# Optimization experiments

Hardware: AMD Instinct MI355X
Metric: run time of the kernel (lower is better)

The kernel has to match this reference:

```python
import jax, jax.numpy as jnp
import numpy as np

NEG_INF = -1e30


def setup_inputs() -> dict:
    key = jax.random.key(0)
    k1, k2, k3 = jax.random.split(key, 3)
    B, H, HKV, S, D = 2, 16, 4, 2048, 128
    q = jax.random.normal(k1, (B, H, S, D), dtype=jnp.float32)
    k = jax.random.normal(k2, (B, HKV, S, D), dtype=jnp.float32)
    v = jax.random.normal(k3, (B, HKV, S, D), dtype=jnp.float32)
    return {"q": q, "k": k, "v": v}


def reference(q, k, v):
    # Flash attention math (exact, non-tiled reference): causal + sliding-window
    # masked softmax(QK^T * scale) V with GQA head grouping.
    B, H, M, D = q.shape
    _, HKV, N, _ = k.shape
    G = H // HKV  # num_kv_groups
    W = 512       # sliding window size
    scale = 1.0 / jnp.sqrt(jnp.float32(D))

    qg = q.reshape(B, HKV, G, M, D)
    # scores: [B, HKV, G, M, N]
    scores = jnp.einsum("bkgmd,bknd->bkgmn", qg, k) * scale

    i = jnp.arange(M)[:, None]
    j = jnp.arange(N)[None, :]
    # causal: j <= i ; sliding window: only last W keys visible (i - j < W)
    keep = (j <= i) & ((i - j) < W)
    scores = jnp.where(keep[None, None, None], scores, NEG_INF)

    p = jax.nn.softmax(scores.astype(jnp.float32), axis=-1).astype(q.dtype)
    out = jnp.einsum("bkgmn,bknd->bkgmd", p, v)
    return out.reshape(B, H, M, D)
```

## Files before the change

kernel.cpp:

```cpp
#include <hip/hip_runtime.h>
#include <hip/hip_bf16.h>
#include <stdint.h>

#define SEQ 2048
#define HD  128
#define WIN 512
#define NH  16
#define NKV 4
#define BATCH 2

typedef __attribute__((ext_vector_type(8))) short bf16x8;
typedef __attribute__((ext_vector_type(4))) float f32x4;

#define EXP2(x) __builtin_amdgcn_exp2f(x)

#define KSTR 136
#define VSTR 72
#define PSTR 72

__device__ __forceinline__ uint32_t pk2(float a, float b) {
    __hip_bfloat162 h = __float22bfloat162_rn(make_float2(a, b));
    return *reinterpret_cast<uint32_t*>(&h);
}
__device__ __forceinline__ uint16_t pk1(float a) {
    __hip_bfloat16 h = __float2bfloat16(a);
    return *reinterpret_cast<uint16_t*>(&h);
}

__global__ __launch_bounds__(256, 2) void fa_mfma(
    const float* __restrict__ q,
    const float* __restrict__ k,
    const float* __restrict__ v,
    float* __restrict__ out)
{
    const int tid  = threadIdx.x;
    const int wave = tid >> 6;
    const int lane = tid & 63;
    const int l4   = lane >> 4;
    const int l15  = lane & 15;

    const int bh   = blockIdx.x >> 4;
    const int qblk = blockIdx.x & 15;
    const int q0   = qblk << 7;
    const int hkv  = (bh & (NH - 1)) >> 2;
    const int b    = bh >> 4;

    const int i0   = q0 + wave * 32;

    __shared__ __align__(16) uint16_t lds_k[64 * KSTR];
    __shared__ __align__(16) uint16_t lds_vt[HD * VSTR];
    __shared__ __align__(16) uint16_t lds_p[4 * 32 * PSTR];
    uint16_t* pw = &lds_p[wave * 32 * PSTR];

    const float scale2 = 0.08838834764831845f * 1.4426950408889634f;

    const size_t qbase  = (size_t)bh * SEQ * HD;
    const size_t kvbase = (size_t)(b * NKV + hkv) * SEQ * HD;

    union { bf16x8 f; uint32_t u[4]; } qf[2][4];
    #pragma unroll
    for (int nt = 0; nt < 2; ++nt) {
        const float* qr = q + qbase + (size_t)(i0 + nt * 16 + l15) * HD;
        #pragma unroll
        for (int ks = 0; ks < 4; ++ks) {
            const float4* g = reinterpret_cast<const float4*>(qr + ks * 32 + l4 * 8);
            float4 a = g[0], bq = g[1];
            qf[nt][ks].u[0] = pk2(a.x * scale2, a.y * scale2);
            qf[nt][ks].u[1] = pk2(a.z * scale2, a.w * scale2);
            qf[nt][ks].u[2] = pk2(bq.x * scale2, bq.y * scale2);
            qf[nt][ks].u[3] = pk2(bq.z * scale2, bq.w * scale2);
        }
    }

    f32x4 O[2][8];
    #pragma unroll
    for (int a1 = 0; a1 < 2; ++a1)
        #pragma unroll
        for (int a2 = 0; a2 < 8; ++a2) O[a1][a2] = (f32x4){0.f, 0.f, 0.f, 0.f};
    float mrow[2] = {-1e30f, -1e30f};
    float lrow[2] = {0.f, 0.f};

    const int kt_lo_blk = (q0 >= 512) ? ((q0 - 511) >> 6) : 0;
    const int kt_hi_blk = (q0 + 127) >> 6;
    const int lo_w = (i0 >= 512) ? ((i0 - 511) >> 6) : 0;
    const int hi_w = (i0 + 31) >> 6;

    const int vdg = tid & 31;
    const int vkg = tid >> 5;
    float4 rKa[4], rKb[4], rV[8];

    auto prefetch = [&](int kt) {
        const float* kp = k + kvbase + (size_t)kt * 64 * HD;
        const float* vp = v + kvbase + (size_t)kt * 64 * HD;
        #pragma unroll
        for (int it = 0; it < 4; ++it) {
            int flat8 = tid + it * 256, key = flat8 >> 4, ch = flat8 & 15;
            const float4* g = reinterpret_cast<const float4*>(kp + key * HD + ch * 8);
            rKa[it] = g[0]; rKb[it] = g[1];
        }
        #pragma unroll
        for (int r = 0; r < 8; ++r)
            rV[r] = *reinterpret_cast<const float4*>(vp + (vkg * 8 + r) * HD + vdg * 4);
    };

    prefetch(kt_lo_blk);

    for (int kt = kt_lo_blk; kt <= kt_hi_blk; ++kt) {
        #pragma unroll
        for (int it = 0; it < 4; ++it) {
            int flat8 = tid + it * 256, key = flat8 >> 4, ch = flat8 & 15;
            uint4 wv;
            wv.x = pk2(rKa[it].x, rKa[it].y);  wv.y = pk2(rKa[it].z, rKa[it].w);
            wv.z = pk2(rKb[it].x, rKb[it].y);  wv.w = pk2(rKb[it].z, rKb[it].w);
            *reinterpret_cast<uint4*>(&lds_k[key * KSTR + ch * 8]) = wv;
        }
        {
            const float* rvf = reinterpret_cast<const float*>(rV);
            #pragma unroll
            for (int i = 0; i < 4; ++i) {
                uint4 wv;
                wv.x = pk2(rvf[0 * 4 + i], rvf[1 * 4 + i]);
                wv.y = pk2(rvf[2 * 4 + i], rvf[3 * 4 + i]);
                wv.z = pk2(rvf[4 * 4 + i], rvf[5 * 4 + i]);
                wv.w = pk2(rvf[6 * 4 + i], rvf[7 * 4 + i]);
                *reinterpret_cast<uint4*>(&lds_vt[(vdg * 4 + i) * VSTR + vkg * 8]) = wv;
            }
        }
        __syncthreads();

        if (kt < kt_hi_blk) prefetch(kt + 1);

        if (kt >= lo_w && kt <= hi_w) {
            f32x4 sf[4][2];
            #pragma unroll
            for (int mt = 0; mt < 4; ++mt) {
                #pragma unroll
                for (int nt = 0; nt < 2; ++nt) sf[mt][nt] = (f32x4){0.f, 0.f, 0.f, 0.f};
                #pragma unroll
                for (int ks = 0; ks < 4; ++ks) {
                    bf16x8 af = *reinterpret_cast<const bf16x8*>(
                        &lds_k[(mt * 16 + l15) * KSTR + ks * 32 + l4 * 8]);
                    #pragma unroll
                    for (int nt = 0; nt < 2; ++nt)
                        sf[mt][nt] = __builtin_amdgcn_mfma_f32_16x16x32_bf16(
                            af, qf[nt][ks].f, sf[mt][nt], 0, 0, 0);
                }
            }
            const bool needmask = (kt == hi_w) || (kt == lo_w && i0 > 511);
            if (needmask) {
                #pragma unroll
                for (int mt = 0; mt < 4; ++mt) {
                    int jb = kt * 64 + mt * 16 + l4 * 4;
                    #pragma unroll
                    for (int nt = 0; nt < 2; ++nt) {
                        int iq = i0 + nt * 16 + l15;
                        #pragma unroll
                        for (int r = 0; r < 4; ++r) {
                            int j = jb + r;
                            if (!((j <= iq) && (iq - j < WIN))) sf[mt][nt][r] = -1e30f;
                        }
                    }
                }
            }
            float alpha[2];
            #pragma unroll
            for (int nt = 0; nt < 2; ++nt) {
                float tm = -1e30f;
                #pragma unroll
                for (int mt = 0; mt < 4; ++mt)
                    #pragma unroll
                    for (int r = 0; r < 4; ++r) tm = fmaxf(tm, sf[mt][nt][r]);
                tm = fmaxf(tm, __shfl_xor(tm, 16, 64));
                tm = fmaxf(tm, __shfl_xor(tm, 32, 64));
                float mn = fmaxf(mrow[nt], tm);
                alpha[nt] = EXP2(mrow[nt] - mn);
                mrow[nt] = mn;
                float me = fmaxf(mn, -1e20f);
                float ts = 0.f;
                #pragma unroll
                for (int mt = 0; mt < 4; ++mt) {
                    #pragma unroll
                    for (int r = 0; r < 4; ++r) {
                        float pv = EXP2(sf[mt][nt][r] - me);
                        ts += pv;
                        pw[(nt * 16 + l15) * PSTR + mt * 16 + l4 * 4 + r] = pk1(pv);
                    }
                }
                ts += __shfl_xor(ts, 16, 64);
                ts += __shfl_xor(ts, 32, 64);
                lrow[nt] = lrow[nt] * alpha[nt] + ts;
            }
            #pragma unroll
            for (int mt = 0; mt < 2; ++mt) {
                #pragma unroll
                for (int r = 0; r < 4; ++r) {
                    float ar = __shfl(alpha[mt], l4 * 4 + r, 64);
                    #pragma unroll
                    for (int nt = 0; nt < 8; ++nt) O[mt][nt][r] *= ar;
                }
            }
            #pragma unroll
            for (int ks = 0; ks < 2; ++ks) {
                bf16x8 pa[2];
                #pragma unroll
                for (int mt = 0; mt < 2; ++mt)
                    pa[mt] = *reinterpret_cast<const bf16x8*>(
                        &pw[(mt * 16 + l15) * PSTR + ks * 32 + l4 * 8]);
                #pragma unroll
                for (int nt = 0; nt < 8; ++nt) {
                    bf16x8 vf = *reinterpret_cast<const bf16x8*>(
                        &lds_vt[(nt * 16 + l15) * VSTR + ks * 32 + l4 * 8]);
                    #pragma unroll
                    for (int mt = 0; mt < 2; ++mt)
                        O[mt][nt] = __builtin_amdgcn_mfma_f32_16x16x32_bf16(
                            pa[mt], vf, O[mt][nt], 0, 0, 0);
                }
            }
        }
        __syncthreads();
    }

    #pragma unroll
    for (int mt = 0; mt < 2; ++mt) {
        float inv = 1.0f / lrow[mt];
        #pragma unroll
        for (int r = 0; r < 4; ++r) {
            float li = __shfl(inv, l4 * 4 + r, 64);
            int row = i0 + mt * 16 + l4 * 4 + r;
            float* orow = out + qbase + (size_t)row * HD;
            #pragma unroll
            for (int nt = 0; nt < 8; ++nt)
                orow[nt * 16 + l15] = O[mt][nt][r] * li;
        }
    }
}

extern "C" void kernel_launch(void* const* d_in, const int* in_sizes, int n_in,
                              void* d_out, int out_size, void* d_ws, size_t ws_size,
                              hipStream_t stream) {
    const float* q = (const float*)d_in[0];
    const float* k = (const float*)d_in[1];
    const float* v = (const float*)d_in[2];
    float* out     = (float*)d_out;

    hipLaunchKernelGGL(fa_mfma, dim3(BATCH * NH * (SEQ / 128)), dim3(256), 0, stream,
                       q, k, v, out);
}
```

Baseline: 126.9 us.

## Double-buffer K/V in LDS, keep P in registers, defer softmax rescaling

Adds two LDS buffers for K and V^T so the next tile is packed while the current one is computed, which removes one barrier per iteration. The probability tile now stays in registers as bf16x4 fragments and feeds 16x16x16 MFMAs directly, replacing the LDS round-trip through lds_p. The O and l rescale is skipped when the new row max exceeds the running max by at most 8 in log2 units, so exponentials may reach up to 256 before normalization. The cost is double the LDS for K/V, more MFMA instructions of the smaller shape, and a small numerical-range risk from the deferred max.

After: 192.4 us. 51.5% more time.

```diff
diff --git a/kernel.cpp b/kernel.cpp
--- a/kernel.cpp
+++ b/kernel.cpp
@@ -10,21 +10,27 @@
 #define BATCH 2
 
 typedef __attribute__((ext_vector_type(8))) short bf16x8;
+typedef __attribute__((ext_vector_type(4))) short bf16x4;
 typedef __attribute__((ext_vector_type(4))) float f32x4;
 
 #define EXP2(x) __builtin_amdgcn_exp2f(x)
 
 #define KSTR 136
 #define VSTR 72
-#define PSTR 72
 
 __device__ __forceinline__ uint32_t pk2(float a, float b) {
     __hip_bfloat162 h = __float22bfloat162_rn(make_float2(a, b));
     return *reinterpret_cast<uint32_t*>(&h);
 }
-__device__ __forceinline__ uint16_t pk1(float a) {
-    __hip_bfloat16 h = __float2bfloat16(a);
-    return *reinterpret_cast<uint16_t*>(&h);
+
+__device__ __forceinline__ f32x4 mfma16(bf16x4 a, bf16x4 b, f32x4 c) {
+#if __has_builtin(__builtin_amdgcn_mfma_f32_16x16x16bf16_1k)
+    return __builtin_amdgcn_mfma_f32_16x16x16bf16_1k(a, b, c, 0, 0, 0);
+#else
+    asm volatile("v_mfma_f32_16x16x16_bf16 %0, %1, %2, %0\n\ts_nop 7\n\ts_nop 7"
+                 : "+v"(c) : "v"(a), "v"(b));
+    return c;
+#endif
 }
 
 __global__ __launch_bounds__(256, 2) void fa_mfma(
@@ -47,10 +53,8 @@
 
     const int i0   = q0 + wave * 32;
 
-    __shared__ __align__(16) uint16_t lds_k[64 * KSTR];
-    __shared__ __align__(16) uint16_t lds_vt[HD * VSTR];
-    __shared__ __align__(16) uint16_t lds_p[4 * 32 * PSTR];
-    uint16_t* pw = &lds_p[wave * 32 * PSTR];
+    __shared__ __align__(16) uint16_t lds_k[2][64 * KSTR];
+    __shared__ __align__(16) uint16_t lds_vt[2][HD * VSTR];
 
     const float scale2 = 0.08838834764831845f * 1.4426950408889634f;
 
@@ -103,32 +107,35 @@
             rV[r] = *reinterpret_cast<const float4*>(vp + (vkg * 8 + r) * HD + vdg * 4);
     };
 
-    prefetch(kt_lo_blk);
-
-    for (int kt = kt_lo_blk; kt <= kt_hi_blk; ++kt) {
+    auto pack = [&](int pb) {
         #pragma unroll
         for (int it = 0; it < 4; ++it) {
             int flat8 = tid + it * 256, key = flat8 >> 4, ch = flat8 & 15;
             uint4 wv;
             wv.x = pk2(rKa[it].x, rKa[it].y);  wv.y = pk2(rKa[it].z, rKa[it].w);
             wv.z = pk2(rKb[it].x, rKb[it].y);  wv.w = pk2(rKb[it].z, rKb[it].w);
-            *reinterpret_cast<uint4*>(&lds_k[key * KSTR + ch * 8]) = wv;
-        }
-        {
-            const float* rvf = reinterpret_cast<const float*>(rV);
-            #pragma unroll
-            for (int i = 0; i < 4; ++i) {
-                uint4 wv;
-                wv.x = pk2(rvf[0 * 4 + i], rvf[1 * 4 + i]);
-                wv.y = pk2(rvf[2 * 4 + i], rvf[3 * 4 + i]);
-                wv.z = pk2(rvf[4 * 4 + i], rvf[5 * 4 + i]);
-                wv.w = pk2(rvf[6 * 4 + i], rvf[7 * 4 + i]);
-                *reinterpret_cast<uint4*>(&lds_vt[(vdg * 4 + i) * VSTR + vkg * 8]) = wv;
-            }
-        }
-        __syncthreads();
-
-        if (kt < kt_hi_blk) prefetch(kt + 1);
+            *reinterpret_cast<uint4*>(&lds_k[pb][key * KSTR + ch * 8]) = wv;
+        }
+        const float* rvf = reinterpret_cast<const float*>(rV);
+        #pragma unroll
+        for (int i = 0; i < 4; ++i) {
+            uint4 wv;
+            wv.x = pk2(rvf[0 * 4 + i], rvf[1 * 4 + i]);
+            wv.y = pk2(rvf[2 * 4 + i], rvf[3 * 4 + i]);
+            wv.z = pk2(rvf[4 * 4 + i], rvf[5 * 4 + i]);
+            wv.w = pk2(rvf[6 * 4 + i], rvf[7 * 4 + i]);
+            *reinterpret_cast<uint4*>(&lds_vt[pb][(vdg * 4 + i) * VSTR + vkg * 8]) = wv;
+        }
+    };
+
+    prefetch(kt_lo_blk);
+    pack(0);
+    __syncthreads();
+
+    int par = 0;
+    for (int kt = kt_lo_blk; kt <= kt_hi_blk; ++kt) {
+        const bool more = (kt < kt_hi_blk);
+        if (more) prefetch(kt + 1);
 
         if (kt >= lo_w && kt <= hi_w) {
             f32x4 sf[4][2];
@@ -139,7 +146,7 @@
                 #pragma unroll
                 for (int ks = 0; ks < 4; ++ks) {
                     bf16x8 af = *reinterpret_cast<const bf16x8*>(
-                        &lds_k[(mt * 16 + l15) * KSTR + ks * 32 + l4 * 8]);
+                        &lds_k[par][(mt * 16 + l15) * KSTR + ks * 32 + l4 * 8]);
                     #pragma unroll
                     for (int nt = 0; nt < 2; ++nt)
                         sf[mt][nt] = __builtin_amdgcn_mfma_f32_16x16x32_bf16(
@@ -162,62 +169,80 @@
                     }
                 }
             }
-            float alpha[2];
+            float tm[2];
             #pragma unroll
             for (int nt = 0; nt < 2; ++nt) {
-                float tm = -1e30f;
-                #pragma unroll
-                for (int mt = 0; mt < 4; ++mt)
-                    #pragma unroll
-                    for (int r = 0; r < 4; ++r) tm = fmaxf(tm, sf[mt][nt][r]);
-                tm = fmaxf(tm, __shfl_xor(tm, 16, 64));
-                tm = fmaxf(tm, __shfl_xor(tm, 32, 64));
-                float mn = fmaxf(mrow[nt], tm);
-                alpha[nt] = EXP2(mrow[nt] - mn);
-                mrow[nt] = mn;
-                float me = fmaxf(mn, -1e20f);
-                float ts = 0.f;
-                #pragma unroll
-                for (int mt = 0; mt < 4; ++mt) {
+                float a0 = fmaxf(fmaxf(sf[0][nt][0], sf[0][nt][1]),
+                                 fmaxf(sf[0][nt][2], sf[0][nt][3]));
+                float a1 = fmaxf(fmaxf(sf[1][nt][0], sf[1][nt][1]),
+                                 fmaxf(sf[1][nt][2], sf[1][nt][3]));
+                float a2 = fmaxf(fmaxf(sf[2][nt][0], sf[2][nt][1]),
+                                 fmaxf(sf[2][nt][2], sf[2][nt][3]));
+                float a3 = fmaxf(fmaxf(sf[3][nt][0], sf[3][nt][1]),
+                                 fmaxf(sf[3][nt][2], sf[3][nt][3]));
+                float t = fmaxf(fmaxf(a0, a1), fmaxf(a2, a3));
+                t = fmaxf(t, __shfl_xor(t, 16, 64));
+                t = fmaxf(t, __shfl_xor(t, 32, 64));
+                tm[nt] = t;
+            }
+            const bool defer = __all(tm[0] <= mrow[0] + 8.0f) &&
+                               __all(tm[1] <= mrow[1] + 8.0f);
+            if (!defer) {
+                float alpha[2];
+                #pragma unroll
+                for (int nt = 0; nt < 2; ++nt) {
+                    float mn = fmaxf(mrow[nt], tm[nt]);
+                    alpha[nt] = EXP2(mrow[nt] - mn);
+                    mrow[nt] = mn;
+                    lrow[nt] *= alpha[nt];
+                }
+                #pragma unroll
+                for (int mt = 0; mt < 2; ++mt) {
                     #pragma unroll
                     for (int r = 0; r < 4; ++r) {
-                        float pv = EXP2(sf[mt][nt][r] - me);
-                        ts += pv;
-                        pw[(nt * 16 + l15) * PSTR + mt * 16 + l4 * 4 + r] = pk1(pv);
+                        float ar = __shfl(alpha[mt], l4 * 4 + r, 64);
+                        #pragma unroll
+                        for (int nt = 0; nt < 8; ++nt) O[mt][nt][r] *= ar;
                     }
                 }
+            }
+            union PF { bf16x4 v; uint32_t u[2]; };
+            PF pfrag[4][2];
+            #pragma unroll
+            for (int nt = 0; nt < 2; ++nt) {
+                float me = fmaxf(mrow[nt], -1e20f);
+                float s[4];
+                #pragma unroll
+                for (int mt = 0; mt < 4; ++mt) {
+                    float p0 = EXP2(sf[mt][nt][0] - me);
+                    float p1 = EXP2(sf[mt][nt][1] - me);
+                    float p2 = EXP2(sf[mt][nt][2] - me);
+                    float p3 = EXP2(sf[mt][nt][3] - me);
+                    pfrag[mt][nt].u[0] = pk2(p0, p1);
+                    pfrag[mt][nt].u[1] = pk2(p2, p3);
+                    s[mt] = (p0 + p1) + (p2 + p3);
+                }
+                float ts = (s[0] + s[1]) + (s[2] + s[3]);
                 ts += __shfl_xor(ts, 16, 64);
                 ts += __shfl_xor(ts, 32, 64);
-                lrow[nt] = lrow[nt] * alpha[nt] + ts;
-            }
-            #pragma unroll
-            for (int mt = 0; mt < 2; ++mt) {
-                #pragma unroll
-                for (int r = 0; r < 4; ++r) {
-                    float ar = __shfl(alpha[mt], l4 * 4 + r, 64);
-                    #pragma unroll
-                    for (int nt = 0; nt < 8; ++nt) O[mt][nt][r] *= ar;
-                }
-            }
-            #pragma unroll
-            for (int ks = 0; ks < 2; ++ks) {
-                bf16x8 pa[2];
-                #pragma unroll
-                for (int mt = 0; mt < 2; ++mt)
-                    pa[mt] = *reinterpret_cast<const bf16x8*>(
-                        &pw[(mt * 16 + l15) * PSTR + ks * 32 + l4 * 8]);
+                lrow[nt] += ts;
+            }
+            if (more) pack(par ^ 1);
+            #pragma unroll
+            for (int mt = 0; mt < 4; ++mt) {
                 #pragma unroll
                 for (int nt = 0; nt < 8; ++nt) {
-                    bf16x8 vf = *reinterpret_cast<const bf16x8*>(
-                        &lds_vt[(nt * 16 + l15) * VSTR + ks * 32 + l4 * 8]);
-                    #pragma unroll
-                    for (int mt = 0; mt < 2; ++mt)
-                        O[mt][nt] = __builtin_amdgcn_mfma_f32_16x16x32_bf16(
-                            pa[mt], vf, O[mt][nt], 0, 0, 0);
-                }
-            }
+                    bf16x4 vf = *reinterpret_cast<const bf16x4*>(
+                        &lds_vt[par][(nt * 16 + l15) * VSTR + mt * 16 + l4 * 4]);
+                    O[0][nt] = mfma16(pfrag[mt][0].v, vf, O[0][nt]);
+                    O[1][nt] = mfma16(pfrag[mt][1].v, vf, O[1][nt]);
+                }
+            }
+        } else {
+            if (more) pack(par ^ 1);
         }
         __syncthreads();
+        par ^= 1;
     }
 
     #pragma unroll
```
